# Optimization experiments

Hardware: AMD Instinct MI355X
Metric: run time of the kernel (lower is better)

The kernel has to match this reference:

```python
import jax, jax.numpy as jnp
import numpy as np

EPS = 1e-6

def _ln(x, g, b):
    m = jnp.mean(x, axis=-1, keepdims=True)
    v = jnp.mean(jnp.square(x - m), axis=-1, keepdims=True)
    return (x - m) * jax.lax.rsqrt(v + EPS) * g + b

def setup_inputs() -> dict:
    key = jax.random.key(0)
    ks = jax.random.split(key, 8)
    B, T, D, K = 512, 1024, 64, 16
    return {
        "z": jax.random.normal(ks[0], (B, T, D), jnp.float32),
        "prototypes": jax.random.normal(ks[1], (K, D), jnp.float32),
        "alphas": jax.random.normal(ks[2], (T, D), jnp.float32),
        "b_bias": jax.random.normal(ks[3], (D,), jnp.float32),
        "W": jax.random.normal(ks[4], (D, D), jnp.float32) / np.sqrt(D),
        "Wb": jax.random.normal(ks[5], (D,), jnp.float32) * 0.02,
        "ln_gamma": jnp.ones((5, D), jnp.float32),
        "ln_beta": jnp.zeros((5, D), jnp.float32),
        "beta_seq": jax.random.normal(ks[6], (K, D), jnp.float32) / np.sqrt(D),
    }

def reference(z, prototypes, alphas, b_bias, W, Wb, ln_gamma, ln_beta, beta_seq):
    # z: [B,T,D], prototypes: [K,D], alphas: [T,D]
    D = z.shape[-1]
    scale = 1.0 / jnp.sqrt(jnp.asarray(D, z.dtype))

    # --- intention_clustering: p_{k|i} ---
    zn = _ln(z, ln_gamma[0], ln_beta[0])                      # [B,T,D]
    pn = _ln(prototypes, ln_gamma[1], ln_beta[1])             # [K,D]
    scores_k = jnp.einsum('btd,kd->btk', zn, pn) * scale      # [B,T,K]
    p_k_i = jax.nn.softmax(scores_k, axis=-1)                 # normalize over intents K

    # --- intention_weighting: p_i ---
    k_ = _ln(alphas + z, ln_gamma[2], ln_beta[2])             # [B,T,D]
    k = k_ + jnp.einsum('btd,de->bte', k_, W) + Wb            # residual Dense
    q = _ln(alphas[-1] + z[:, -1] + b_bias, ln_gamma[3], ln_beta[3])  # [B,D] last-position query
    scores_t = jnp.einsum('btd,bd->bt', k, q) * scale         # [B,T]
    p_i = jax.nn.softmax(scores_t, axis=1)                    # normalize over positions T

    # --- intention_aggr ---
    w = p_k_i * p_i[..., None]                                # [B,T,K]
    out = jnp.einsum('btk,btd->bkd', w, z)                    # [B,K,D]
    return _ln(beta_seq + out, ln_gamma[4], ln_beta[4])       # [B,K,D]
```

## Files before the change

### kernel.cpp

```cpp
#include <hip/hip_runtime.h>
#include <math.h>

#define EPSF   1e-6f
#define SCALE  0.125f
#define NEG_HUGE -3.402823466e38f

#define PW_STRIDE 4104

__device__ __forceinline__ float rs_nr(float x) {
    float r = rsqrtf(x);
    return r * (1.5f - 0.5f * x * r * r);
}

__device__ __forceinline__ float dot4(float4 a, float4 b) {
    return fmaf(a.x, b.x, fmaf(a.y, b.y, fmaf(a.z, b.z, a.w * b.w)));
}

extern "C" __global__ __launch_bounds__(1024, 8)
void disent_encoder_kernel(const float* __restrict__ z,
                           const float* __restrict__ proto,
                           const float* __restrict__ alphas,
                           const float* __restrict__ b_bias,
                           const float* __restrict__ W,
                           const float* __restrict__ Wb,
                           const float* __restrict__ lng,
                           const float* __restrict__ lnb,
                           const float* __restrict__ beta_seq,
                           float* __restrict__ out)
{
    const int b    = blockIdx.x;
    const int tid  = threadIdx.x;
    const int lane = tid & 63;
    const int wid  = tid >> 6;

    __shared__ __align__(16) float s_pw[4 * PW_STRIDE];
    __shared__ __align__(16) float s_GP[16 * 64];
    __shared__ __align__(16) float s_G2Q[64];
    __shared__ float s_sGP[16];
    __shared__ float s_BP[16];
    __shared__ float s_red[20];
    __shared__ float s_c[2];

    const float* zb = z + (size_t)b * 1024 * 64;

    if (wid == 0) {
        int d = lane;
        float a = alphas[1023 * 64 + d] + zb[1023 * 64 + d] + b_bias[d];
        float s1 = a, s2 = a * a;
#pragma unroll
        for (int off = 32; off >= 1; off >>= 1) {
            s1 += __shfl_xor(s1, off);
            s2 += __shfl_xor(s2, off);
        }
        float m  = s1 * (1.f / 64.f);
        float v  = s2 * (1.f / 64.f) - m * m;
        float rs = rs_nr(v + EPSF);
        float qd = fmaf((a - m) * rs, lng[3*64 + d], lnb[3*64 + d]);
        float s = 0.f;
#pragma unroll 4
        for (int eq = 0; eq < 16; ++eq) {
            float4 w4 = *(const float4*)&W[d*64 + eq*4];
            s = fmaf(w4.x, __shfl(qd, 4*eq+0),
                fmaf(w4.y, __shfl(qd, 4*eq+1),
                fmaf(w4.z, __shfl(qd, 4*eq+2),
                fmaf(w4.w, __shfl(qd, 4*eq+3), s))));
        }
        float qpp  = qd + s;
        float G2Qd = lng[2*64 + d] * qpp;
        s_G2Q[d] = G2Qd;
        float r1 = G2Qd;
        float r2 = fmaf(lnb[2*64 + d], qpp, Wb[d] * qd);
#pragma unroll
        for (int off = 32; off >= 1; off >>= 1) {
            r1 += __shfl_xor(r1, off);
            r2 += __shfl_xor(r2, off);
        }
        if (d == 0) { s_c[0] = r1; s_c[1] = r2; }
    } else if (wid == 1 && lane < 16) {
        int k = lane;
        float s1 = 0.f, s2 = 0.f;
#pragma unroll 4
        for (int qd = 0; qd < 16; ++qd) {
            float4 p = *(const float4*)&proto[k*64 + qd*4];
            s1 += (p.x + p.y) + (p.z + p.w);
            s2 += dot4(p, p);
        }
        float m  = s1 * (1.f / 64.f);
        float v  = s2 * (1.f / 64.f) - m * m;
        float rs = rs_nr(v + EPSF);
        float sgp = 0.f, bp = 0.f;
        for (int d2 = 0; d2 < 64; ++d2) {
            float pn = fmaf((proto[k*64 + d2] - m) * rs, lng[64 + d2], lnb[64 + d2]);
            float gp = lng[d2] * pn;
            s_GP[k*64 + d2] = gp;
            sgp += gp;
            bp = fmaf(lnb[d2], pn, bp);
        }
        s_sGP[k] = sgp;
        s_BP[k]  = bp;
    }
    __syncthreads();

    const float sG2Q = s_c[0];
    const float TQc  = s_c[1];

    float st, se;
    float sk[16];
    {
        const int t = tid;
        const float4* zp = (const float4*)(zb + (size_t)t * 64);
        const float4* ap = (const float4*)(alphas + (size_t)t * 64);
        float dk[16];
#pragma unroll
        for (int k = 0; k < 16; ++k) dk[k] = 0.f;
        float sz = 0.f, szz = 0.f, sa = 0.f, saa = 0.f, da = 0.f;

#pragma unroll 4
        for (int qd = 0; qd < 16; ++qd) {
            float4 gq = *(const float4*)&s_G2Q[qd*4];
            float4 zq = zp[qd];
            float4 aq = ap[qd];
            float ux = zq.x + aq.x, uy = zq.y + aq.y;
            float uz = zq.z + aq.z, uw = zq.w + aq.w;
            sz  += (zq.x + zq.y) + (zq.z + zq.w);
            szz  = fmaf(zq.x, zq.x, fmaf(zq.y, zq.y,
                   fmaf(zq.z, zq.z, fmaf(zq.w, zq.w, szz))));
            sa  += (ux + uy) + (uz + uw);
            saa  = fmaf(ux, ux, fmaf(uy, uy, fmaf(uz, uz, fmaf(uw, uw, saa))));
            da   = fmaf(ux, gq.x, fmaf(uy, gq.y, fmaf(uz, gq.z, fmaf(uw, gq.w, da))));
#pragma unroll
            for (int k = 0; k < 16; ++k) {
                float4 g = *(const float4*)&s_GP[k*64 + qd*4];
                dk[k] = fmaf(zq.x, g.x, fmaf(zq.y, g.y,
                        fmaf(zq.z, g.z, fmaf(zq.w, g.w, dk[k]))));
            }
        }

        float m    = sz  * (1.f / 64.f);
        float var  = szz * (1.f / 64.f) - m * m;
        float rs   = rs_nr(var + EPSF);
        float ma   = sa  * (1.f / 64.f);
        float vara = saa * (1.f / 64.f) - ma * ma;
        float rsa  = rs_nr(vara + EPSF);

        st = (rsa * (da - ma * sG2Q) + TQc) * SCALE;

        float mx = NEG_HUGE;
#pragma unroll
        for (int k = 0; k < 16; ++k) {
            float s = (rs * (dk[k] - m * s_sGP[k]) + s_BP[k]) * SCALE;
            sk[k] = s;
            mx = fmaxf(mx, s);
        }
        se = 0.f;
#pragma unroll
        for (int k = 0; k < 16; ++k) { sk[k] = __expf(sk[k] - mx); se += sk[k]; }
    }

    float lm = st;
#pragma unroll
    for (int off = 32; off >= 1; off >>= 1) lm = fmaxf(lm, __shfl_xor(lm, off));
    if (lane == 0) s_red[wid] = lm;
    __syncthreads();
    if (tid == 0) {
        float m0 = s_red[0];
#pragma unroll
        for (int w = 1; w < 16; ++w) m0 = fmaxf(m0, s_red[w]);
        s_red[16] = m0;
    }
    __syncthreads();
    float M  = s_red[16];
    float e0 = __expf(st - M);
    float ls = e0;
#pragma unroll
    for (int off = 32; off >= 1; off >>= 1) ls += __shfl_xor(ls, off);
    if (lane == 0) s_red[wid] = ls;
    __syncthreads();
    if (tid == 0) {
        float s0 = 0.f;
#pragma unroll
        for (int w = 0; w < 16; ++w) s0 += s_red[w];
        s_red[17] = 1.f / s0;
    }
    __syncthreads();
    float invZ = s_red[17];

    {
        float c0 = (e0 * invZ) / se;
#pragma unroll
        for (int kq = 0; kq < 4; ++kq) {
            float4 w0 = make_float4(sk[4*kq+0]*c0, sk[4*kq+1]*c0,
                                    sk[4*kq+2]*c0, sk[4*kq+3]*c0);
            *(float4*)&s_pw[kq*PW_STRIDE + tid*4] = w0;
        }
    }
    __syncthreads();

    const int kq = lane >> 4;
    const int dq = lane & 15;
    float acc[4][4];
#pragma unroll
    for (int i = 0; i < 4; ++i)
#pragma unroll
        for (int j = 0; j < 4; ++j) acc[i][j] = 0.f;

    const int tb = wid * 64;
#pragma unroll 4
    for (int tt = 0; tt < 64; ++tt) {
        int t = tb + tt;
        float4 zq = *(const float4*)&zb[(size_t)t*64 + dq*4];
        float4 wq = *(const float4*)&s_pw[kq*PW_STRIDE + t*4];
        float zv[4] = { zq.x, zq.y, zq.z, zq.w };
        float wv[4] = { wq.x, wq.y, wq.z, wq.w };
#pragma unroll
        for (int i = 0; i < 4; ++i)
#pragma unroll
            for (int j = 0; j < 4; ++j)
                acc[i][j] = fmaf(wv[i], zv[j], acc[i][j]);
    }
    __syncthreads();

    float* s_part = s_pw;
#pragma unroll
    for (int i = 0; i < 4; ++i) {
        float4 v = make_float4(acc[i][0], acc[i][1], acc[i][2], acc[i][3]);
        *(float4*)&s_part[wid*1024 + (kq*4 + i)*64 + dq*4] = v;
    }
    __syncthreads();

    if (tid < 256) {
        int k  = tid >> 4;
        int dg = tid & 15;
        float4 v = make_float4(0.f, 0.f, 0.f, 0.f);
#pragma unroll
        for (int w = 0; w < 16; ++w) {
            float4 p = *(const float4*)&s_part[w*1024 + k*64 + dg*4];
            v.x += p.x; v.y += p.y; v.z += p.z; v.w += p.w;
        }
        float4 bs = *(const float4*)&beta_seq[k*64 + dg*4];
        v.x += bs.x; v.y += bs.y; v.z += bs.z; v.w += bs.w;

        float s1 = (v.x + v.y) + (v.z + v.w);
        float s2 = dot4(v, v);
#pragma unroll
        for (int off = 1; off <= 8; off <<= 1) {
            s1 += __shfl_xor(s1, off);
            s2 += __shfl_xor(s2, off);
        }
        float m   = s1 * (1.f / 64.f);
        float var = s2 * (1.f / 64.f) - m * m;
        float rs  = rs_nr(var + EPSF);
        float4 g4 = *(const float4*)&lng[4*64 + dg*4];
        float4 b4 = *(const float4*)&lnb[4*64 + dg*4];
        float4 o;
        o.x = fmaf((v.x - m) * rs, g4.x, b4.x);
        o.y = fmaf((v.y - m) * rs, g4.y, b4.y);
        o.z = fmaf((v.z - m) * rs, g4.z, b4.z);
        o.w = fmaf((v.w - m) * rs, g4.w, b4.w);
        *(float4*)&out[((size_t)b*16 + k)*64 + dg*4] = o;
    }
}

extern "C" void kernel_launch(void* const* d_in, const int* in_sizes, int n_in,
                              void* d_out, int out_size, void* d_ws, size_t ws_size,
                              hipStream_t stream) {
    const float* z        = (const float*)d_in[0];
    const float* proto    = (const float*)d_in[1];
    const float* alphas   = (const float*)d_in[2];
    const float* b_bias   = (const float*)d_in[3];
    const float* W        = (const float*)d_in[4];
    const float* Wb       = (const float*)d_in[5];
    const float* lng      = (const float*)d_in[6];
    const float* lnb      = (const float*)d_in[7];
    const float* beta_seq = (const float*)d_in[8];
    float* out = (float*)d_out;

    disent_encoder_kernel<<<dim3(512), dim3(1024), 0, stream>>>(
        z, proto, alphas, b_bias, W, Wb, lng, lnb, beta_seq, out);
}
```

Before: 293.9 us.

## Split fused encoder kernel into five kernels with finer-grained grids

Replaces the single 1024-thread-per-batch kernel with a pipeline: a prologue computes per-batch query terms and the prototype projection, a scores kernel computes positional scores, a softmax kernel normalises them, an aggregation kernel splits T into four slices with partial sums, and a final kernel reduces the partials and applies layernorm. The aim is more, smaller blocks for better occupancy and less block-wide synchronisation. In exchange z is read twice from memory, intermediates go through global workspace, and there are extra launch overheads.

```diff
diff --git a/kernel.cpp b/kernel.cpp
--- a/kernel.cpp
+++ b/kernel.cpp
@@ -5,55 +5,66 @@
 #define SCALE  0.125f
 #define NEG_HUGE -3.402823466e38f
 
-#define PW_STRIDE 4104
+#define PW_STRIDE 1032
+
+#define WS_SCORES 0
+#define WS_PI     (512*1024)
+#define WS_PART   (2*512*1024)
+#define WS_GP     (WS_PART + 512*4*16*64)
+#define WS_SGPBP  (WS_GP + 16*64)
+#define WS_G2Q    (WS_SGPBP + 32)
+#define WS_CPAIR  (WS_G2Q + 512*64)
 
 __device__ __forceinline__ float rs_nr(float x) {
     float r = rsqrtf(x);
     return r * (1.5f - 0.5f * x * r * r);
 }
 
-__device__ __forceinline__ float dot4(float4 a, float4 b) {
-    return fmaf(a.x, b.x, fmaf(a.y, b.y, fmaf(a.z, b.z, a.w * b.w)));
-}
-
-extern "C" __global__ __launch_bounds__(1024, 8)
-void disent_encoder_kernel(const float* __restrict__ z,
-                           const float* __restrict__ proto,
-                           const float* __restrict__ alphas,
-                           const float* __restrict__ b_bias,
-                           const float* __restrict__ W,
-                           const float* __restrict__ Wb,
-                           const float* __restrict__ lng,
-                           const float* __restrict__ lnb,
-                           const float* __restrict__ beta_seq,
-                           float* __restrict__ out)
-{
-    const int b    = blockIdx.x;
-    const int tid  = threadIdx.x;
-    const int lane = tid & 63;
-    const int wid  = tid >> 6;
-
-    __shared__ __align__(16) float s_pw[4 * PW_STRIDE];
-    __shared__ __align__(16) float s_GP[16 * 64];
-    __shared__ __align__(16) float s_G2Q[64];
-    __shared__ float s_sGP[16];
-    __shared__ float s_BP[16];
-    __shared__ float s_red[20];
-    __shared__ float s_c[2];
-
-    const float* zb = z + (size_t)b * 1024 * 64;
-
-    if (wid == 0) {
-        int d = lane;
-        float a = alphas[1023 * 64 + d] + zb[1023 * 64 + d] + b_bias[d];
-        float s1 = a, s2 = a * a;
+__global__ __launch_bounds__(64)
+void k0_prologue(const float* __restrict__ z, const float* __restrict__ proto,
+                 const float* __restrict__ alphas, const float* __restrict__ b_bias,
+                 const float* __restrict__ W, const float* __restrict__ Wb,
+                 const float* __restrict__ lng, const float* __restrict__ lnb,
+                 float* __restrict__ ws)
+{
+    const int lane = threadIdx.x;
+    if (blockIdx.x == 512) {
+        if (lane < 16) {
+            const int k = lane;
+            float s1 = 0.f, s2 = 0.f;
+#pragma unroll 4
+            for (int qd = 0; qd < 16; ++qd) {
+                float4 p = *(const float4*)&proto[k*64 + qd*4];
+                s1 += (p.x + p.y) + (p.z + p.w);
+                s2 = fmaf(p.x,p.x, fmaf(p.y,p.y, fmaf(p.z,p.z, fmaf(p.w,p.w, s2))));
+            }
+            float m  = s1 * (1.f/64.f);
+            float v  = s2 * (1.f/64.f) - m*m;
+            float rs = rs_nr(v + EPSF);
+            float sgp = 0.f, bp = 0.f;
+            for (int d = 0; d < 64; ++d) {
+                float pn = fmaf((proto[k*64 + d] - m) * rs, lng[64 + d], lnb[64 + d]);
+                float g  = lng[d] * pn;
+                ws[WS_GP + k*64 + d] = g;
+                sgp += g;
+                bp = fmaf(lnb[d], pn, bp);
+            }
+            ws[WS_SGPBP + k]      = sgp;
+            ws[WS_SGPBP + 16 + k] = bp;
+        }
+    } else {
+        const int b = blockIdx.x;
+        const int d = lane;
+        const float* zb = z + (size_t)b * 65536;
+        float a = alphas[1023*64 + d] + zb[1023*64 + d] + b_bias[d];
+        float s1 = a, s2 = a*a;
 #pragma unroll
         for (int off = 32; off >= 1; off >>= 1) {
             s1 += __shfl_xor(s1, off);
             s2 += __shfl_xor(s2, off);
         }
-        float m  = s1 * (1.f / 64.f);
-        float v  = s2 * (1.f / 64.f) - m * m;
+        float m  = s1 * (1.f/64.f);
+        float v  = s2 * (1.f/64.f) - m*m;
         float rs = rs_nr(v + EPSF);
         float qd = fmaf((a - m) * rs, lng[3*64 + d], lnb[3*64 + d]);
         float s = 0.f;
@@ -67,7 +78,7 @@
         }
         float qpp  = qd + s;
         float G2Qd = lng[2*64 + d] * qpp;
-        s_G2Q[d] = G2Qd;
+        ws[WS_G2Q + b*64 + d] = G2Qd;
         float r1 = G2Qd;
         float r2 = fmaf(lnb[2*64 + d], qpp, Wb[d] * qd);
 #pragma unroll
@@ -75,123 +86,132 @@
             r1 += __shfl_xor(r1, off);
             r2 += __shfl_xor(r2, off);
         }
-        if (d == 0) { s_c[0] = r1; s_c[1] = r2; }
-    } else if (wid == 1 && lane < 16) {
-        int k = lane;
-        float s1 = 0.f, s2 = 0.f;
-#pragma unroll 4
+        if (d == 0) { ws[WS_CPAIR + b*2] = r1; ws[WS_CPAIR + b*2 + 1] = r2; }
+    }
+}
+
+__global__ __launch_bounds__(256, 8)
+void k1_scores(const float* __restrict__ z, const float* __restrict__ alphas,
+               const float* __restrict__ ws_ro, float* __restrict__ ws)
+{
+    const int b     = blockIdx.x >> 4;
+    const int slice = blockIdx.x & 15;
+    const int tid   = threadIdx.x;
+    const int qg    = tid & 3;
+    const int t     = slice*64 + (tid >> 2);
+    const float* zb = z + (size_t)b * 65536;
+
+    const float sG2Q = ws_ro[WS_CPAIR + b*2];
+    const float TQc  = ws_ro[WS_CPAIR + b*2 + 1];
+    const float* g2qb = ws_ro + WS_G2Q + b*64;
+
+    float sa = 0.f, saa = 0.f, da = 0.f;
+#pragma unroll
+    for (int i = 0; i < 4; ++i) {
+        const int qd = qg + i*4;
+        float4 zq = *(const float4*)&zb[(size_t)t*64 + qd*4];
+        float4 aq = *(const float4*)&alphas[(size_t)t*64 + qd*4];
+        float4 gq = *(const float4*)&g2qb[qd*4];
+        float ux = zq.x+aq.x, uy = zq.y+aq.y, uz = zq.z+aq.z, uw = zq.w+aq.w;
+        sa += (ux+uy)+(uz+uw);
+        saa = fmaf(ux,ux, fmaf(uy,uy, fmaf(uz,uz, fmaf(uw,uw, saa))));
+        da  = fmaf(ux,gq.x, fmaf(uy,gq.y, fmaf(uz,gq.z, fmaf(uw,gq.w, da))));
+    }
+    sa  += __shfl_xor(sa, 1);  sa  += __shfl_xor(sa, 2);
+    saa += __shfl_xor(saa, 1); saa += __shfl_xor(saa, 2);
+    da  += __shfl_xor(da, 1);  da  += __shfl_xor(da, 2);
+
+    float ma   = sa  * (1.f/64.f);
+    float vara = saa * (1.f/64.f) - ma*ma;
+    float rsa  = rs_nr(vara + EPSF);
+    float st   = (rsa * (da - ma * sG2Q) + TQc) * SCALE;
+    if (qg == 0) ws[WS_SCORES + b*1024 + t] = st;
+}
+
+__global__ __launch_bounds__(256, 8)
+void k2_softmax(const float* __restrict__ ws_ro, float* __restrict__ ws)
+{
+    const int b = blockIdx.x;
+    const int tid = threadIdx.x, lane = tid & 63, wid = tid >> 6;
+    __shared__ float s_red[6];
+    float4 s4 = *(const float4*)&ws_ro[WS_SCORES + b*1024 + tid*4];
+    float lm = fmaxf(fmaxf(s4.x, s4.y), fmaxf(s4.z, s4.w));
+#pragma unroll
+    for (int off = 32; off >= 1; off >>= 1) lm = fmaxf(lm, __shfl_xor(lm, off));
+    if (lane == 0) s_red[wid] = lm;
+    __syncthreads();
+    if (tid == 0)
+        s_red[4] = fmaxf(fmaxf(s_red[0], s_red[1]), fmaxf(s_red[2], s_red[3]));
+    __syncthreads();
+    float M = s_red[4];
+    float e0 = __expf(s4.x - M), e1 = __expf(s4.y - M);
+    float e2 = __expf(s4.z - M), e3 = __expf(s4.w - M);
+    float ls = (e0 + e1) + (e2 + e3);
+#pragma unroll
+    for (int off = 32; off >= 1; off >>= 1) ls += __shfl_xor(ls, off);
+    if (lane == 0) s_red[wid] = ls;
+    __syncthreads();
+    if (tid == 0) s_red[5] = 1.f / (s_red[0] + s_red[1] + s_red[2] + s_red[3]);
+    __syncthreads();
+    float invZ = s_red[5];
+    *(float4*)&ws[WS_PI + b*1024 + tid*4] =
+        make_float4(e0*invZ, e1*invZ, e2*invZ, e3*invZ);
+}
+
+__global__ __launch_bounds__(256, 8)
+void k3_aggr(const float* __restrict__ z, const float* __restrict__ ws_ro,
+             float* __restrict__ ws)
+{
+    const int b     = blockIdx.x >> 2;
+    const int slice = blockIdx.x & 3;
+    const int tid   = threadIdx.x;
+    const int lane  = tid & 63;
+    const int wid   = tid >> 6;
+    const int tbase = slice * 256;
+    const float* zb = z + (size_t)b * 65536;
+    const float* gp = ws_ro + WS_GP;
+
+    __shared__ __align__(16) float s_pw[4 * PW_STRIDE];
+
+    const float pi_t = ws_ro[WS_PI + b*1024 + tbase + tid];
+    {
+        const float4* zp = (const float4*)(zb + (size_t)(tbase + tid) * 64);
+        float dk[16];
+#pragma unroll
+        for (int k = 0; k < 16; ++k) dk[k] = 0.f;
+        float sz = 0.f, szz = 0.f;
+#pragma unroll 2
         for (int qd = 0; qd < 16; ++qd) {
-            float4 p = *(const float4*)&proto[k*64 + qd*4];
-            s1 += (p.x + p.y) + (p.z + p.w);
-            s2 += dot4(p, p);
-        }
-        float m  = s1 * (1.f / 64.f);
-        float v  = s2 * (1.f / 64.f) - m * m;
-        float rs = rs_nr(v + EPSF);
-        float sgp = 0.f, bp = 0.f;
-        for (int d2 = 0; d2 < 64; ++d2) {
-            float pn = fmaf((proto[k*64 + d2] - m) * rs, lng[64 + d2], lnb[64 + d2]);
-            float gp = lng[d2] * pn;
-            s_GP[k*64 + d2] = gp;
-            sgp += gp;
-            bp = fmaf(lnb[d2], pn, bp);
-        }
-        s_sGP[k] = sgp;
-        s_BP[k]  = bp;
-    }
-    __syncthreads();
-
-    const float sG2Q = s_c[0];
-    const float TQc  = s_c[1];
-
-    float st, se;
-    float sk[16];
-    {
-        const int t = tid;
-        const float4* zp = (const float4*)(zb + (size_t)t * 64);
-        const float4* ap = (const float4*)(alphas + (size_t)t * 64);
-        float dk[16];
-#pragma unroll
-        for (int k = 0; k < 16; ++k) dk[k] = 0.f;
-        float sz = 0.f, szz = 0.f, sa = 0.f, saa = 0.f, da = 0.f;
-
-#pragma unroll 4
-        for (int qd = 0; qd < 16; ++qd) {
-            float4 gq = *(const float4*)&s_G2Q[qd*4];
             float4 zq = zp[qd];
-            float4 aq = ap[qd];
-            float ux = zq.x + aq.x, uy = zq.y + aq.y;
-            float uz = zq.z + aq.z, uw = zq.w + aq.w;
-            sz  += (zq.x + zq.y) + (zq.z + zq.w);
-            szz  = fmaf(zq.x, zq.x, fmaf(zq.y, zq.y,
-                   fmaf(zq.z, zq.z, fmaf(zq.w, zq.w, szz))));
-            sa  += (ux + uy) + (uz + uw);
-            saa  = fmaf(ux, ux, fmaf(uy, uy, fmaf(uz, uz, fmaf(uw, uw, saa))));
-            da   = fmaf(ux, gq.x, fmaf(uy, gq.y, fmaf(uz, gq.z, fmaf(uw, gq.w, da))));
+            sz += (zq.x + zq.y) + (zq.z + zq.w);
+            szz = fmaf(zq.x,zq.x, fmaf(zq.y,zq.y, fmaf(zq.z,zq.z, fmaf(zq.w,zq.w, szz))));
 #pragma unroll
             for (int k = 0; k < 16; ++k) {
-                float4 g = *(const float4*)&s_GP[k*64 + qd*4];
-                dk[k] = fmaf(zq.x, g.x, fmaf(zq.y, g.y,
-                        fmaf(zq.z, g.z, fmaf(zq.w, g.w, dk[k]))));
+                float4 g = *(const float4*)&gp[k*64 + qd*4];
+                dk[k] = fmaf(zq.x,g.x, fmaf(zq.y,g.y,
+                        fmaf(zq.z,g.z, fmaf(zq.w,g.w, dk[k]))));
             }
         }
-
-        float m    = sz  * (1.f / 64.f);
-        float var  = szz * (1.f / 64.f) - m * m;
-        float rs   = rs_nr(var + EPSF);
-        float ma   = sa  * (1.f / 64.f);
-        float vara = saa * (1.f / 64.f) - ma * ma;
-        float rsa  = rs_nr(vara + EPSF);
-
-        st = (rsa * (da - ma * sG2Q) + TQc) * SCALE;
-
+        float m   = sz  * (1.f/64.f);
+        float var = szz * (1.f/64.f) - m*m;
+        float rs  = rs_nr(var + EPSF);
+        float sk[16];
         float mx = NEG_HUGE;
 #pragma unroll
         for (int k = 0; k < 16; ++k) {
-            float s = (rs * (dk[k] - m * s_sGP[k]) + s_BP[k]) * SCALE;
+            float s = (rs * (dk[k] - m * ws_ro[WS_SGPBP + k]) + ws_ro[WS_SGPBP + 16 + k]) * SCALE;
             sk[k] = s;
             mx = fmaxf(mx, s);
         }
-        se = 0.f;
+        float se = 0.f;
 #pragma unroll
         for (int k = 0; k < 16; ++k) { sk[k] = __expf(sk[k] - mx); se += sk[k]; }
-    }
-
-    float lm = st;
-#pragma unroll
-    for (int off = 32; off >= 1; off >>= 1) lm = fmaxf(lm, __shfl_xor(lm, off));
-    if (lane == 0) s_red[wid] = lm;
-    __syncthreads();
-    if (tid == 0) {
-        float m0 = s_red[0];
-#pragma unroll
-        for (int w = 1; w < 16; ++w) m0 = fmaxf(m0, s_red[w]);
-        s_red[16] = m0;
-    }
-    __syncthreads();
-    float M  = s_red[16];
-    float e0 = __expf(st - M);
-    float ls = e0;
-#pragma unroll
-    for (int off = 32; off >= 1; off >>= 1) ls += __shfl_xor(ls, off);
-    if (lane == 0) s_red[wid] = ls;
-    __syncthreads();
-    if (tid == 0) {
-        float s0 = 0.f;
-#pragma unroll
-        for (int w = 0; w < 16; ++w) s0 += s_red[w];
-        s_red[17] = 1.f / s0;
-    }
-    __syncthreads();
-    float invZ = s_red[17];
-
-    {
-        float c0 = (e0 * invZ) / se;
+        const float c = pi_t / se;
 #pragma unroll
         for (int kq = 0; kq < 4; ++kq) {
-            float4 w0 = make_float4(sk[4*kq+0]*c0, sk[4*kq+1]*c0,
-                                    sk[4*kq+2]*c0, sk[4*kq+3]*c0);
-            *(float4*)&s_pw[kq*PW_STRIDE + tid*4] = w0;
+            float4 w4 = make_float4(sk[4*kq+0]*c, sk[4*kq+1]*c,
+                                    sk[4*kq+2]*c, sk[4*kq+3]*c);
+            *(float4*)&s_pw[kq*PW_STRIDE + tid*4] = w4;
         }
     }
     __syncthreads();
@@ -204,12 +224,11 @@
 #pragma unroll
         for (int j = 0; j < 4; ++j) acc[i][j] = 0.f;
 
-    const int tb = wid * 64;
 #pragma unroll 4
     for (int tt = 0; tt < 64; ++tt) {
-        int t = tb + tt;
-        float4 zq = *(const float4*)&zb[(size_t)t*64 + dq*4];
-        float4 wq = *(const float4*)&s_pw[kq*PW_STRIDE + t*4];
+        const int tl = wid*64 + tt;
+        float4 zq = *(const float4*)&zb[(size_t)(tbase + tl)*64 + dq*4];
+        float4 wq = *(const float4*)&s_pw[kq*PW_STRIDE + tl*4];
         float zv[4] = { zq.x, zq.y, zq.z, zq.w };
         float wv[4] = { wq.x, wq.y, wq.z, wq.w };
 #pragma unroll
@@ -228,37 +247,55 @@
     }
     __syncthreads();
 
-    if (tid < 256) {
-        int k  = tid >> 4;
-        int dg = tid & 15;
+    {
+        const int k  = tid >> 4;
+        const int dg = tid & 15;
         float4 v = make_float4(0.f, 0.f, 0.f, 0.f);
 #pragma unroll
-        for (int w = 0; w < 16; ++w) {
+        for (int w = 0; w < 4; ++w) {
             float4 p = *(const float4*)&s_part[w*1024 + k*64 + dg*4];
             v.x += p.x; v.y += p.y; v.z += p.z; v.w += p.w;
         }
-        float4 bs = *(const float4*)&beta_seq[k*64 + dg*4];
-        v.x += bs.x; v.y += bs.y; v.z += bs.z; v.w += bs.w;
-
-        float s1 = (v.x + v.y) + (v.z + v.w);
-        float s2 = dot4(v, v);
-#pragma unroll
-        for (int off = 1; off <= 8; off <<= 1) {
-            s1 += __shfl_xor(s1, off);
-            s2 += __shfl_xor(s2, off);
-        }
-        float m   = s1 * (1.f / 64.f);
-        float var = s2 * (1.f / 64.f) - m * m;
-        float rs  = rs_nr(var + EPSF);
-        float4 g4 = *(const float4*)&lng[4*64 + dg*4];
-        float4 b4 = *(const float4*)&lnb[4*64 + dg*4];
-        float4 o;
-        o.x = fmaf((v.x - m) * rs, g4.x, b4.x);
-        o.y = fmaf((v.y - m) * rs, g4.y, b4.y);
-        o.z = fmaf((v.z - m) * rs, g4.z, b4.z);
-        o.w = fmaf((v.w - m) * rs, g4.w, b4.w);
-        *(float4*)&out[((size_t)b*16 + k)*64 + dg*4] = o;
-    }
+        *(float4*)&ws[WS_PART + (((size_t)b*4 + slice)*16 + k)*64 + dg*4] = v;
+    }
+}
+
+__global__ __launch_bounds__(256, 8)
+void k4_final(const float* __restrict__ ws_ro, const float* __restrict__ beta_seq,
+              const float* __restrict__ lng, const float* __restrict__ lnb,
+              float* __restrict__ out)
+{
+    const int b   = blockIdx.x;
+    const int tid = threadIdx.x;
+    const int k   = tid >> 4;
+    const int dg  = tid & 15;
+    float4 v = make_float4(0.f, 0.f, 0.f, 0.f);
+#pragma unroll
+    for (int s = 0; s < 4; ++s) {
+        float4 p = *(const float4*)&ws_ro[WS_PART + (((size_t)b*4 + s)*16 + k)*64 + dg*4];
+        v.x += p.x; v.y += p.y; v.z += p.z; v.w += p.w;
+    }
+    float4 bs = *(const float4*)&beta_seq[k*64 + dg*4];
+    v.x += bs.x; v.y += bs.y; v.z += bs.z; v.w += bs.w;
+
+    float s1 = (v.x + v.y) + (v.z + v.w);
+    float s2 = fmaf(v.x,v.x, fmaf(v.y,v.y, fmaf(v.z,v.z, v.w*v.w)));
+#pragma unroll
+    for (int off = 1; off <= 8; off <<= 1) {
+        s1 += __shfl_xor(s1, off);
+        s2 += __shfl_xor(s2, off);
+    }
+    float m   = s1 * (1.f/64.f);
+    float var = s2 * (1.f/64.f) - m*m;
+    float rs  = rs_nr(var + EPSF);
+    float4 g4 = *(const float4*)&lng[4*64 + dg*4];
+    float4 b4 = *(const float4*)&lnb[4*64 + dg*4];
+    float4 o;
+    o.x = fmaf((v.x - m)*rs, g4.x, b4.x);
+    o.y = fmaf((v.y - m)*rs, g4.y, b4.y);
+    o.z = fmaf((v.z - m)*rs, g4.z, b4.z);
+    o.w = fmaf((v.w - m)*rs, g4.w, b4.w);
+    *(float4*)&out[((size_t)b*16 + k)*64 + dg*4] = o;
 }
 
 extern "C" void kernel_launch(void* const* d_in, const int* in_sizes, int n_in,
@@ -274,7 +311,12 @@
     const float* lnb      = (const float*)d_in[7];
     const float* beta_seq = (const float*)d_in[8];
     float* out = (float*)d_out;
-
-    disent_encoder_kernel<<<dim3(512), dim3(1024), 0, stream>>>(
-        z, proto, alphas, b_bias, W, Wb, lng, lnb, beta_seq, out);
-}
+    float* ws  = (float*)d_ws;
+
+    k0_prologue<<<dim3(513),  dim3(64),  0, stream>>>(z, proto, alphas, b_bias,
+                                                      W, Wb, lng, lnb, ws);
+    k1_scores  <<<dim3(8192), dim3(256), 0, stream>>>(z, alphas, ws, ws);
+    k2_softmax <<<dim3(512),  dim3(256), 0, stream>>>(ws, ws);
+    k3_aggr    <<<dim3(2048), dim3(256), 0, stream>>>(z, ws, ws);
+    k4_final   <<<dim3(512),  dim3(256), 0, stream>>>(ws, beta_seq, lng, lnb, out);
+}
```

Measured after the change: 290.1 us. About the same (-1.3%).
